# Kernel optimization log

Measured on AMD Instinct MI355X. Metric: run time of the kernel, lower is better.

The kernel has to match this reference:

```python
import jax, jax.numpy as jnp
import numpy as np
import math

T, B, D = 1024, 256, 64
E, H, L = 512, 256, 4


def setup_inputs() -> dict:
    key = jax.random.key(0)
    ks = jax.random.split(key, 10)
    x_sequence = jax.random.normal(ks[0], (T, B, D), dtype=jnp.float32)
    seq_lengths = jax.random.randint(ks[1], (B,), 1, T)
    # create_b_mask: ones in first half of dims, zeros in second half
    b_mask = jnp.concatenate([jnp.ones((1, D // 2)), jnp.zeros((1, D // 2))], axis=1).astype(jnp.float32)
    W_in = jax.random.normal(ks[2], (L, D + E, H), dtype=jnp.float32) / np.sqrt(D + E)
    b_in = jnp.zeros((L, H), dtype=jnp.float32)
    W_s = jax.random.normal(ks[3], (L, H, D), dtype=jnp.float32) / np.sqrt(H)
    b_s = jnp.zeros((L, D), dtype=jnp.float32)
    W_t = jax.random.normal(ks[4], (L, H, D), dtype=jnp.float32) / np.sqrt(H)
    b_t = jnp.zeros((L, D), dtype=jnp.float32)
    rescale_w = jnp.ones((1, D), dtype=jnp.float32)
    # ESN reservoir (fixed random), scaled for spectral stability under tanh
    W_res = jax.random.normal(ks[5], (E, E), dtype=jnp.float32) * (0.9 / np.sqrt(E))
    W_inp = jax.random.normal(ks[6], (D, E), dtype=jnp.float32) * 0.1
    return dict(x_sequence=x_sequence, seq_lengths=seq_lengths, b_mask=b_mask,
                W_in=W_in, b_in=b_in, W_s=W_s, b_s=b_s, W_t=W_t, b_t=b_t,
                rescale_w=rescale_w, W_res=W_res, W_inp=W_inp)


def _forward(x_sequence, seq_lengths, b_mask, W_in, b_in, W_s, b_s, W_t, b_t,
             rescale_w, W_res, W_inp):
    Tlen, Bsz, Dd = x_sequence.shape
    log2pi = jnp.asarray(math.log(2.0 * math.pi), dtype=x_sequence.dtype)

    def nn_apply(xm, h_esn, l):
        # small conditioning MLP: concat(masked frame, esn state) -> hidden -> (slope, intercept)
        inp = jnp.concatenate([xm, h_esn], axis=1)           # (B, D+E)
        hid = jnp.tanh(inp @ W_in[l] + b_in[l])              # (B, H)
        slope = jnp.tanh(hid @ W_s[l] + b_s[l]) * rescale_w  # (B, D), rescaled
        intercept = hid @ W_t[l] + b_t[l]                    # (B, D)
        return slope, intercept

    def f_inverse(z, m, h_esn, l):
        slope, intercept = nn_apply(m * z, h_esn, l)
        z_new = m * z + (1.0 - m) * ((z - intercept) * jnp.exp(-slope))
        log_det = slope @ (m.T - 1.0)                        # (B, 1)
        return z_new, log_det

    def loglike_frame(x_frame, h_esn):
        ll = jnp.zeros((Bsz, 1), dtype=x_frame.dtype)
        z = x_frame
        for l in reversed(range(L)):  # small fixed loop over flow layers
            z, ld = f_inverse(z, 1.0 - b_mask, h_esn, l)
            ll = ll + ld
            z, ld = f_inverse(z, b_mask, h_esn, l)
            ll = ll + ld
        ll = ll - 0.5 * jnp.sum(z * z, axis=1, keepdims=True) - 0.5 * Dd * log2pi
        return ll

    def step(carry, inp):
        h_esn, ll_seq = carry
        t, x_frame = inp
        lf = loglike_frame(x_frame, h_esn)
        length_mask = (t < seq_lengths).astype(lf.dtype)[:, None]  # (B,1)
        ll_seq = ll_seq + lf * length_mask
        h_esn = jnp.tanh(h_esn @ W_res.T + x_frame @ W_inp)        # ESN update
        return (h_esn, ll_seq), None

    h0 = jnp.zeros((Bsz, W_res.shape[0]), dtype=x_sequence.dtype)
    ll0 = jnp.zeros((Bsz, 1), dtype=x_sequence.dtype)
    ts = jnp.arange(Tlen)
    (h_final, ll_seq), _ = jax.lax.scan(step, (h0, ll0), (ts, x_sequence))
    return ll_seq  # (B, 1)


def reference(x_sequence, seq_lengths, b_mask, W_in, b_in, W_s, b_s, W_t, b_t,
              rescale_w, W_res, W_inp):
    return _forward(x_sequence, seq_lengths, b_mask, W_in, b_in, W_s, b_s,
                    W_t, b_t, rescale_w, W_res, W_inp)
```

## Files before the change

kernel.cpp:

```cpp
#include <hip/hip_runtime.h>

#define T_LEN 1024
#define B_SZ  256
#define D_DIM 64
#define E_DIM 512
#define H_DIM 256

#define SA 552
#define SH 264
#define SF 66
#define ROWB 1152

#define FLOW_LDS (32*SA*2 + 32*SH*2 + 32*4)

using short8 = __attribute__((ext_vector_type(8))) short;
using half8  = __attribute__((ext_vector_type(8))) _Float16;
using f32x4  = __attribute__((ext_vector_type(4))) float;
typedef unsigned long long ull;

static __device__ __forceinline__ unsigned short f2bf(float v) {
    unsigned u = __float_as_uint(v);
    u += 0x7FFFu + ((u >> 16) & 1u);
    return (unsigned short)(u >> 16);
}
static __device__ __forceinline__ unsigned short f2h(float v) {
    _Float16 h = (_Float16)v;
    unsigned short u;
    __builtin_memcpy(&u, &h, 2);
    return u;
}
static __device__ __forceinline__ float h2f(unsigned short u) {
    _Float16 h;
    __builtin_memcpy(&h, &u, 2);
    return (float)h;
}
static __device__ __forceinline__ float fast_tanh(float x) {
    x = fminf(15.f, fmaxf(-15.f, x));
    float e = __expf(2.f * x);
    return (e - 1.f) / (e + 1.f);
}
static __device__ __forceinline__ int rswz(int row, int byte_in_row) {
    return row * ROWB + (byte_in_row ^ ((row & 7) << 4));
}

__global__ void prep_kernel(const float* __restrict__ W_in, const float* __restrict__ W_s,
                            const float* __restrict__ W_t, const float* __restrict__ W_res,
                            const float* __restrict__ W_inp, const float* __restrict__ x_seq,
                            unsigned short* __restrict__ W_inF, unsigned short* __restrict__ W_stF,
                            unsigned short* __restrict__ W_packo, unsigned short* __restrict__ x_h) {
    int idx = blockIdx.x * blockDim.x + threadIdx.x;
    int stride = gridDim.x * blockDim.x;
    const int total1 = 8 * 16 * 17 * 64 * 8;
    for (int i = idx; i < total1; i += stride) {
        int j    = i & 7;
        int lane = (i >> 3) & 63;
        int ks   = (i >> 9) % 17;
        int nt   = (i / (512 * 17)) & 15;
        int ls   = i / (512 * 17 * 16);
        int side = ls & 1, l = ls >> 1;
        int n = nt * 16 + (lane & 15);
        int k = ks * 32 + (lane >> 4) * 8 + j;
        int ksrc = (k < 32) ? (side == 0 ? 32 + k : k) : (k + 32);
        W_inF[i] = f2bf(W_in[(l * 576 + ksrc) * H_DIM + n]);
    }
    const int total2 = 8 * 4 * 8 * 64 * 8;
    for (int i = idx; i < total2; i += stride) {
        int j    = i & 7;
        int lane = (i >> 3) & 63;
        int ks   = (i >> 9) & 7;
        int nt   = (i >> 12) & 3;
        int ls   = i >> 14;
        int side = ls & 1, l = ls >> 1;
        int nst = nt * 16 + (lane & 15);
        int k   = ks * 32 + (lane >> 4) * 8 + j;
        int j32 = nst & 31;
        int d   = side ? (32 + j32) : j32;
        float v = (nst < 32) ? W_s[(l * H_DIM + k) * D_DIM + d] : W_t[(l * H_DIM + k) * D_DIM + d];
        W_stF[i] = f2bf(v);
    }
    const int total3 = E_DIM * 576;
    for (int i = idx; i < total3; i += stride) {
        int k = i % 576;
        int n = i / 576;
        float v = (k < E_DIM) ? W_res[n * E_DIM + k] : W_inp[(k - E_DIM) * E_DIM + n];
        W_packo[i] = f2h(v);
    }
    const int total4 = T_LEN * B_SZ * D_DIM;
    for (int i = idx; i < total4; i += stride)
        x_h[i] = f2h(x_seq[i]);
}

__launch_bounds__(256, 1)
__global__ void esn_kernel(const unsigned short* __restrict__ x_h,
                           const unsigned short* __restrict__ W_pack,
                           unsigned short* __restrict__ h_store ,
                           unsigned short* __restrict__ h_buf   ,
                           unsigned int* __restrict__ ctr,
                           int t0, int tc) {
    const int bid  = blockIdx.x;
    const int g    = bid & 15;
    const int m    = bid >> 4;
    const int tid  = threadIdx.x;
    const int wave = tid >> 6;
    const int lane = tid & 63;
    const int arow = lane & 15;
    const int kq   = lane >> 4;
    const int r0   = g * 16;
    const int n0   = m * 64;
    const size_t HB = (size_t)B_SZ * E_DIM;
    unsigned int* gctr = ctr + g * 32;

    extern __shared__ char smem[];
    char* Wlb = smem;
    char* hAb = smem + 64 * ROWB;

    {
        const int r  = tid & 63;
        const int c0 = (tid >> 6) * 18;
        #pragma unroll
        for (int u = 0; u < 18; ++u) {
            const int byte = 16 * (c0 + u);
            *reinterpret_cast<uint4*>(Wlb + rswz(r, byte)) =
                *reinterpret_cast<const uint4*>(
                    reinterpret_cast<const char*>(&W_pack[(size_t)(n0 + r) * 576]) + byte);
        }
    }

    const int srow = tid >> 4;
    const int seg  = tid & 15;
    const int xrow = tid >> 2, xc = tid & 3;

    for (int tl = 0; tl < tc; ++tl) {
        const int t = t0 + tl;
        const unsigned short* hb_r = h_buf + (size_t)(t & 1) * HB;
        unsigned short*       hb_w = h_buf + (size_t)((t & 1) ^ 1) * HB;

        uint4 xa = {0,0,0,0}, xb = {0,0,0,0};
        if (tid < 64) {
            const unsigned short* xp = &x_h[((size_t)t * B_SZ + r0 + xrow) * D_DIM + xc * 16];
            xa = *reinterpret_cast<const uint4*>(xp);
            xb = *reinterpret_cast<const uint4*>(xp + 8);
        }

        if (tid == 0) {
            while (__hip_atomic_fetch_add(gctr, 0u, __ATOMIC_RELAXED,
                                          __HIP_MEMORY_SCOPE_AGENT) < 8u * (unsigned)t)
                __builtin_amdgcn_s_sleep(1);
        }
        __syncthreads();
        asm volatile("" ::: "memory");

        ull hv[8];
        const ull* hrow = reinterpret_cast<const ull*>(&hb_r[(size_t)(r0 + srow) * E_DIM]);
        #pragma unroll
        for (int q = 0; q < 4; ++q) {
            const int c = seg + 16 * q;
            hv[2*q]   = __hip_atomic_load(hrow + 2*c,     __ATOMIC_RELAXED, __HIP_MEMORY_SCOPE_SYSTEM);
            hv[2*q+1] = __hip_atomic_load(hrow + 2*c + 1, __ATOMIC_RELAXED, __HIP_MEMORY_SCOPE_SYSTEM);
        }
        #pragma unroll
        for (int q = 0; q < 4; ++q) {
            const int c = seg + 16 * q;
            uint4 pk;
            __builtin_memcpy(&pk, &hv[2*q], 16);
            *reinterpret_cast<uint4*>(hAb + rswz(srow, 16 * c)) = pk;
        }
        if (tid < 64) {
            *reinterpret_cast<uint4*>(hAb + rswz(xrow, 1024 + 32 * xc))      = xa;
            *reinterpret_cast<uint4*>(hAb + rswz(xrow, 1024 + 32 * xc + 16)) = xb;
        }
        __syncthreads();

        if (tl == 0) {
            #pragma unroll
            for (int q = 0; q < 4; ++q) {
                const int c = seg + 16 * q;
                unsigned short o[8];
                #pragma unroll
                for (int j = 0; j < 4; ++j) o[j]     = f2bf(h2f((unsigned short)(hv[2*q]   >> (16 * j))));
                #pragma unroll
                for (int j = 0; j < 4; ++j) o[4 + j] = f2bf(h2f((unsigned short)(hv[2*q+1] >> (16 * j))));
                uint4 pk;
                __builtin_memcpy(&pk, o, 16);
                *reinterpret_cast<uint4*>(&h_store[(size_t)(r0 + srow) * E_DIM + 8 * c]) = pk;
            }
        }

        f32x4 accA = (f32x4){0.f, 0.f, 0.f, 0.f};
        f32x4 accB = (f32x4){0.f, 0.f, 0.f, 0.f};
        #pragma unroll
        for (int ks = 0; ks < 18; ++ks) {
            half8 a = *reinterpret_cast<const half8*>(hAb + rswz(arow, ks * 64 + kq * 16));
            half8 b = *reinterpret_cast<const half8*>(Wlb + rswz(wave * 16 + arow, ks * 64 + kq * 16));
            if (ks & 1) accB = __builtin_amdgcn_mfma_f32_16x16x32_f16(a, b, accB, 0, 0, 0);
            else        accA = __builtin_amdgcn_mfma_f32_16x16x32_f16(a, b, accA, 0, 0, 0);
        }
        f32x4 acc = accA + accB;

        const int ncol = n0 + wave * 16 + arow;
        #pragma unroll
        for (int i = 0; i < 4; ++i) {
            const int row = r0 + kq * 4 + i;
            float hvf = fast_tanh(acc[i]);
            __hip_atomic_store(&hb_w[(size_t)row * E_DIM + ncol], f2h(hvf),
                               __ATOMIC_RELAXED, __HIP_MEMORY_SCOPE_SYSTEM);
            if (tl + 1 < tc)
                h_store[((size_t)(tl + 1) * B_SZ + row) * E_DIM + ncol] = f2bf(hvf);
        }

        asm volatile("s_waitcnt vmcnt(0)" ::: "memory");
        __syncthreads();
        if (tid == 0)
            __hip_atomic_fetch_add(gctr, 1u, __ATOMIC_RELAXED, __HIP_MEMORY_SCOPE_AGENT);
    }
}

__launch_bounds__(256, 3)
__global__ void flow_kernel(const float* __restrict__ x_seq, const unsigned short* __restrict__ h_store,
                            const unsigned short* __restrict__ W_inF, const unsigned short* __restrict__ W_stF,
                            const float* __restrict__ b_in, const float* __restrict__ b_s,
                            const float* __restrict__ b_t, const float* __restrict__ rescale_w,
                            const int* __restrict__ seq_len, float* __restrict__ ll_part,
                            int t0, int tc) {
    const int ttb  = blockIdx.x >> 4;
    const int bt   = blockIdx.x & 15;
    const int tid  = threadIdx.x;
    const int wave = tid >> 6;
    const int lane = tid & 63;

    extern __shared__ char smemf[];
    unsigned short* abf   = reinterpret_cast<unsigned short*>(smemf);
    unsigned short* hidbf = abf + 32 * SA;
    float* llacc = reinterpret_cast<float*>(hidbf + 32 * SH);
    float* stf   = reinterpret_cast<float*>(hidbf);

    const int r8 = tid >> 3;
    const int c8 = tid & 7;

    const int trow = ttb * 2 + (r8 >> 4);
    const int brow = bt * 16 + (r8 & 15);

    float z[8];
    {
        const float* xp = &x_seq[((size_t)(t0 + trow) * B_SZ + brow) * D_DIM + c8 * 8];
        float4 v0 = *reinterpret_cast<const float4*>(xp);
        float4 v1 = *reinterpret_cast<const float4*>(xp + 4);
        z[0] = v0.x; z[1] = v0.y; z[2] = v0.z; z[3] = v0.w;
        z[4] = v1.x; z[5] = v1.y; z[6] = v1.z; z[7] = v1.w;
        const unsigned short* hp = &h_store[((size_t)trow * B_SZ + brow) * E_DIM + c8 * 64];
        unsigned short* ap = &abf[r8 * SA + 32 + c8 * 64];
        #pragma unroll
        for (int q = 0; q < 8; ++q)
            *reinterpret_cast<uint4*>(ap + q * 8) = *reinterpret_cast<const uint4*>(hp + q * 8);
    }
    if (tid < 32) llacc[tid] = 0.f;
    __syncthreads();

    for (int stage = 0; stage < 8; ++stage) {
        const int l = 3 - (stage >> 1);
        const int side = stage & 1;
        const int ls = l * 2 + side;

        {
            const bool act = side ? (c8 < 4) : (c8 >= 4);
            if (act) {
                unsigned short o[8];
                #pragma unroll
                for (int q = 0; q < 8; ++q) o[q] = f2bf(z[q]);
                const int k = side ? (c8 * 8) : ((c8 - 4) * 8);
                uint4 pk;
                __builtin_memcpy(&pk, o, 16);
                *reinterpret_cast<uint4*>(&abf[r8 * SA + k]) = pk;
            }
        }
        __syncthreads();

        const unsigned short* wbase =
            W_inF + ((size_t)(ls * 16 + wave * 4) * 17) * 512 + lane * 8;
        f32x4 acc[2][4];
        #pragma unroll
        for (int mt = 0; mt < 2; ++mt)
            #pragma unroll
            for (int nt = 0; nt < 4; ++nt)
                acc[mt][nt] = (f32x4){0.f, 0.f, 0.f, 0.f};
        const int aoff = (lane & 15) * SA + 8 * (lane >> 4);
        short8 bb[6][4];
        #pragma unroll
        for (int p = 0; p < 6; ++p)
            #pragma unroll
            for (int nt = 0; nt < 4; ++nt)
                bb[p][nt] = *reinterpret_cast<const short8*>(wbase + (size_t)nt * 8704 + p * 512);
        #pragma unroll
        for (int ks = 0; ks < 17; ++ks) {
            const int k0 = ks * 32;
            short8 a0 = *reinterpret_cast<const short8*>(&abf[aoff + k0]);
            short8 a1 = *reinterpret_cast<const short8*>(&abf[16 * SA + aoff + k0]);
            #pragma unroll
            for (int nt = 0; nt < 4; ++nt) {
                acc[0][nt] = __builtin_amdgcn_mfma_f32_16x16x32_bf16(a0, bb[ks % 6][nt], acc[0][nt], 0, 0, 0);
                acc[1][nt] = __builtin_amdgcn_mfma_f32_16x16x32_bf16(a1, bb[ks % 6][nt], acc[1][nt], 0, 0, 0);
            }
            if (ks + 6 < 17) {
                #pragma unroll
                for (int nt = 0; nt < 4; ++nt)
                    bb[ks % 6][nt] = *reinterpret_cast<const short8*>(
                        wbase + (size_t)nt * 8704 + (ks + 6) * 512);
            }
        }
        #pragma unroll
        for (int mt = 0; mt < 2; ++mt)
            #pragma unroll
            for (int nt = 0; nt < 4; ++nt) {
                const int n = wave * 64 + nt * 16 + (lane & 15);
                const float bias = b_in[l * H_DIM + n];
                #pragma unroll
                for (int i = 0; i < 4; ++i) {
                    const int row = mt * 16 + (lane >> 4) * 4 + i;
                    hidbf[row * SH + n] = f2bf(fast_tanh(acc[mt][nt][i] + bias));
                }
            }
        __syncthreads();

        const unsigned short* wstb =
            W_stF + ((size_t)(ls * 4 + wave) * 8) * 512 + lane * 8;
        f32x4 acc2[2];
        acc2[0] = (f32x4){0.f,0.f,0.f,0.f};
        acc2[1] = (f32x4){0.f,0.f,0.f,0.f};
        const int hoff = (lane & 15) * SH + 8 * (lane >> 4);
        const int nst  = wave * 16 + (lane & 15);
        short8 bs0 = *reinterpret_cast<const short8*>(wstb);
        #pragma unroll
        for (int ks = 0; ks < 8; ++ks) {
            short8 bcur = bs0;
            if (ks + 1 < 8) bs0 = *reinterpret_cast<const short8*>(wstb + (ks + 1) * 512);
            const int k0 = ks * 32;
            short8 a0 = *reinterpret_cast<const short8*>(&hidbf[hoff + k0]);
            short8 a1 = *reinterpret_cast<const short8*>(&hidbf[16 * SH + hoff + k0]);
            acc2[0] = __builtin_amdgcn_mfma_f32_16x16x32_bf16(a0, bcur, acc2[0], 0, 0, 0);
            acc2[1] = __builtin_amdgcn_mfma_f32_16x16x32_bf16(a1, bcur, acc2[1], 0, 0, 0);
        }
        __syncthreads();
        {
            const int j = nst & 31;
            const int d = side ? (32 + j) : j;
            const bool is_s = (nst < 32);
            const float bias = is_s ? b_s[l * D_DIM + d] : b_t[l * D_DIM + d];
            const float rs = rescale_w[d];
            #pragma unroll
            for (int mt = 0; mt < 2; ++mt)
                #pragma unroll
                for (int i = 0; i < 4; ++i) {
                    const int row = mt * 16 + (lane >> 4) * 4 + i;
                    const float v = acc2[mt][i] + bias;
                    stf[row * SF + nst] = is_s ? (fast_tanh(v) * rs) : v;
                }
        }
        __syncthreads();
        {
            const bool act = side ? (c8 >= 4) : (c8 < 4);
            if (act) {
                const int jb = (c8 & 3) * 8;
                float p = 0.f;
                #pragma unroll
                for (int q = 0; q < 8; ++q) {
                    const float sv = stf[r8 * SF + jb + q];
                    const float iv = stf[r8 * SF + 32 + jb + q];
                    z[q] = (z[q] - iv) * __expf(-sv);
                    p += sv;
                }
                p += __shfl_xor(p, 1);
                p += __shfl_xor(p, 2);
                if ((c8 & 3) == 0) llacc[r8] -= p;
            }
        }
    }

    __syncthreads();
    {
        float zs = 0.f;
        #pragma unroll
        for (int q = 0; q < 8; ++q) zs += z[q] * z[q];
        zs += __shfl_xor(zs, 1);
        zs += __shfl_xor(zs, 2);
        zs += __shfl_xor(zs, 4);
        if (c8 == 0) {
            float ll = llacc[r8] - 0.5f * zs - 58.812066125f;
            llacc[r8] = ((t0 + trow) < seq_len[brow]) ? ll : 0.f;
        }
    }
    __syncthreads();
    if (tid < 16)
        ll_part[((size_t)((t0 >> 1) + ttb)) * B_SZ + bt * 16 + tid] =
            llacc[tid] + llacc[16 + tid];
}

__global__ void reduce_kernel(const float* __restrict__ ll_part, float* __restrict__ out) {
    int b = threadIdx.x;
    float s = 0.f;
    #pragma unroll
    for (int tt = 0; tt < T_LEN / 2; ++tt) s += ll_part[tt * B_SZ + b];
    out[b] = s;
}

extern "C" void kernel_launch(void* const* d_in, const int* in_sizes, int n_in,
                              void* d_out, int out_size, void* d_ws, size_t ws_size,
                              hipStream_t stream) {
    const float* x_seq   = (const float*)d_in[0];
    const int*   seqlen  = (const int*)d_in[1];
    const float* W_in    = (const float*)d_in[3];
    const float* b_in    = (const float*)d_in[4];
    const float* W_s     = (const float*)d_in[5];
    const float* b_s     = (const float*)d_in[6];
    const float* W_t     = (const float*)d_in[7];
    const float* b_t     = (const float*)d_in[8];
    const float* rescale = (const float*)d_in[9];
    const float* W_res   = (const float*)d_in[10];
    const float* W_inp   = (const float*)d_in[11];

    char* ws = (char*)d_ws;
    size_t off = 0;
    unsigned short* W_inF  = (unsigned short*)(ws + off); off += (size_t)8 * 16 * 17 * 64 * 8 * 2;
    unsigned short* W_stF  = (unsigned short*)(ws + off); off += (size_t)8 * 4 * 8 * 64 * 8 * 2;
    unsigned short* W_pack = (unsigned short*)(ws + off); off += (size_t)E_DIM * 576 * 2;
    unsigned short* x_h    = (unsigned short*)(ws + off); off += (size_t)T_LEN * B_SZ * D_DIM * 2;
    float* ll_part = (float*)(ws + off); off += (size_t)(T_LEN / 2) * B_SZ * 4;
    unsigned short* h_buf  = (unsigned short*)(ws + off); off += (size_t)2 * B_SZ * E_DIM * 2;
    unsigned int* ctr = (unsigned int*)(ws + off); off += (size_t)16 * 32 * 4;
    unsigned short* h_store = (unsigned short*)(ws + off);

    size_t per_t = (size_t)B_SZ * E_DIM * 2;
    size_t rem = (ws_size > off) ? (ws_size - off) : 0;
    long long tcl = (long long)(rem / per_t);
    int tc = (int)((tcl > T_LEN) ? T_LEN : tcl);
    tc &= ~15;
    if (tc < 16) tc = 16;

    hipMemsetAsync(h_buf, 0, (size_t)2 * B_SZ * E_DIM * 2, stream);
    hipMemsetAsync(ctr, 0, (size_t)16 * 32 * 4, stream);

    prep_kernel<<<2048, 256, 0, stream>>>(W_in, W_s, W_t, W_res, W_inp, x_seq,
                                          W_inF, W_stF, W_pack, x_h);
    const int esn_lds = (64 + 16) * ROWB;
    for (int t0 = 0; t0 < T_LEN; t0 += tc) {
        int cur = T_LEN - t0; if (cur > tc) cur = tc;
        esn_kernel<<<128, 256, esn_lds, stream>>>(x_h, W_pack, h_store, h_buf, ctr, t0, cur);
        flow_kernel<<<(cur / 2) * 16, 256, FLOW_LDS, stream>>>(x_seq, h_store, W_inF, W_stF,
                                                               b_in, b_s, b_t, rescale, seqlen,
                                                               ll_part, t0, cur);
    }
    reduce_kernel<<<1, B_SZ, 0, stream>>>(ll_part, (float*)d_out);
}
```

Before: 3.615 ms.

## Interleave two row groups per ESN block to hide cross-block sync latency

Each ESN workgroup now handles two 16-row batch groups instead of one, and the grid shrinks from 128 to 64 blocks. The block alternates between the groups: while it computes the MFMA and tanh for one group, it waits on the counter and loads the next h state and x frame for the other. This is meant to hide the latency of the global spin-wait and the h_buf loads behind useful compute on the recurrent critical path. The cost is half as many blocks, so each block does twice the serial work, plus a more complex vmcnt-based wait scheme that could deadlock or read stale data if the ordering assumptions are wrong.

```diff
diff --git a/kernel.cpp b/kernel.cpp
--- a/kernel.cpp
+++ b/kernel.cpp
@@ -12,6 +12,7 @@
 #define ROWB 1152
 
 #define FLOW_LDS (32*SA*2 + 32*SH*2 + 32*4)
+#define ESN_LDS  (96*ROWB)
 
 using short8 = __attribute__((ext_vector_type(8))) short;
 using half8  = __attribute__((ext_vector_type(8))) _Float16;
@@ -90,6 +91,96 @@
         x_h[i] = f2h(x_seq[i]);
 }
 
+static __device__ __forceinline__ void esn_phase(
+        char* ha, char* Wlb, int r0x, unsigned int* gcx,
+        ull (&hvx)[8], uint2& xvx,
+        int r0o, unsigned int* gco, ull (&hvo)[8], uint2& xvo,
+        int t, int tl, int tc, int tread, bool do_reads,
+        const unsigned short* __restrict__ x_h,
+        unsigned short* __restrict__ h_store,
+        unsigned short* __restrict__ h_buf,
+        int tid, int wave, int lane, int n0) {
+    const int arow = lane & 15;
+    const int kq   = lane >> 4;
+    const int srow = tid >> 4;
+    const int seg  = tid & 15;
+    const size_t HB = (size_t)B_SZ * E_DIM;
+
+    #pragma unroll
+    for (int qq = 0; qq < 4; ++qq) {
+        const int c = seg + 16 * qq;
+        uint4 pk;
+        __builtin_memcpy(&pk, &hvx[2 * qq], 16);
+        *reinterpret_cast<uint4*>(ha + rswz(srow, 16 * c)) = pk;
+    }
+    *reinterpret_cast<uint2*>(ha + rswz(srow, 1024 + seg * 8)) = xvx;
+    __syncthreads();
+
+    if (tl == 0) {
+        #pragma unroll
+        for (int qq = 0; qq < 4; ++qq) {
+            const int c = seg + 16 * qq;
+            unsigned short o[8];
+            #pragma unroll
+            for (int j = 0; j < 4; ++j) o[j]     = f2bf(h2f((unsigned short)(hvx[2*qq]   >> (16 * j))));
+            #pragma unroll
+            for (int j = 0; j < 4; ++j) o[4 + j] = f2bf(h2f((unsigned short)(hvx[2*qq+1] >> (16 * j))));
+            uint4 pk;
+            __builtin_memcpy(&pk, o, 16);
+            *reinterpret_cast<uint4*>(&h_store[(size_t)(r0x + srow) * E_DIM + 8 * c]) = pk;
+        }
+    }
+
+    f32x4 accA = (f32x4){0.f, 0.f, 0.f, 0.f};
+    f32x4 accB = (f32x4){0.f, 0.f, 0.f, 0.f};
+    #pragma unroll
+    for (int ks = 0; ks < 18; ++ks) {
+        half8 a = *reinterpret_cast<const half8*>(ha + rswz(arow, ks * 64 + kq * 16));
+        half8 b = *reinterpret_cast<const half8*>(Wlb + rswz(wave * 16 + arow, ks * 64 + kq * 16));
+        if (ks & 1) accB = __builtin_amdgcn_mfma_f32_16x16x32_f16(a, b, accB, 0, 0, 0);
+        else        accA = __builtin_amdgcn_mfma_f32_16x16x32_f16(a, b, accA, 0, 0, 0);
+    }
+    f32x4 acc = accA + accB;
+
+    unsigned short* hb_w = h_buf + (size_t)((t + 1) & 1) * HB;
+    const int ncol = n0 + wave * 16 + arow;
+    #pragma unroll
+    for (int i = 0; i < 4; ++i) {
+        const int row = r0x + kq * 4 + i;
+        float hvf = fast_tanh(acc[i]);
+        __hip_atomic_store(&hb_w[(size_t)row * E_DIM + ncol], f2h(hvf),
+                           __ATOMIC_RELAXED, __HIP_MEMORY_SCOPE_SYSTEM);
+        if (tl + 1 < tc)
+            h_store[((size_t)(tl + 1) * B_SZ + row) * E_DIM + ncol] = f2bf(hvf);
+    }
+
+    if (do_reads) {
+        if (tid == 0) {
+            while (__hip_atomic_fetch_add(gco, 0u, __ATOMIC_RELAXED,
+                                          __HIP_MEMORY_SCOPE_AGENT) < 8u * (unsigned)tread)
+                __builtin_amdgcn_s_sleep(1);
+        }
+        __syncthreads();
+        asm volatile("" ::: "memory");
+        const unsigned short* hb_r = h_buf + (size_t)(tread & 1) * HB;
+        const ull* hrow = reinterpret_cast<const ull*>(&hb_r[(size_t)(r0o + srow) * E_DIM]);
+        #pragma unroll
+        for (int qq = 0; qq < 4; ++qq) {
+            const int c = seg + 16 * qq;
+            hvo[2*qq]   = __hip_atomic_load(hrow + 2*c,     __ATOMIC_RELAXED, __HIP_MEMORY_SCOPE_SYSTEM);
+            hvo[2*qq+1] = __hip_atomic_load(hrow + 2*c + 1, __ATOMIC_RELAXED, __HIP_MEMORY_SCOPE_SYSTEM);
+        }
+        xvo = *reinterpret_cast<const uint2*>(
+            &x_h[((size_t)tread * B_SZ + r0o + srow) * D_DIM + seg * 4]);
+        asm volatile("s_waitcnt vmcnt(9)" ::: "memory");
+    } else {
+        asm volatile("s_waitcnt vmcnt(0)" ::: "memory");
+    }
+    __syncthreads();
+    if (tid == 0)
+        __hip_atomic_fetch_add(gcx, 1u, __ATOMIC_RELAXED, __HIP_MEMORY_SCOPE_AGENT);
+}
+
 __launch_bounds__(256, 1)
 __global__ void esn_kernel(const unsigned short* __restrict__ x_h,
                            const unsigned short* __restrict__ W_pack,
@@ -98,21 +189,23 @@
                            unsigned int* __restrict__ ctr,
                            int t0, int tc) {
     const int bid  = blockIdx.x;
-    const int g    = bid & 15;
-    const int m    = bid >> 4;
+    const int q    = bid & 7;
+    const int m    = bid >> 3;
     const int tid  = threadIdx.x;
     const int wave = tid >> 6;
     const int lane = tid & 63;
-    const int arow = lane & 15;
-    const int kq   = lane >> 4;
-    const int r0   = g * 16;
     const int n0   = m * 64;
     const size_t HB = (size_t)B_SZ * E_DIM;
-    unsigned int* gctr = ctr + g * 32;
+
+    const int r0A = (q * 2) * 16;
+    const int r0B = (q * 2 + 1) * 16;
+    unsigned int* gcA = ctr + (q * 2) * 32;
+    unsigned int* gcB = ctr + (q * 2 + 1) * 32;
 
     extern __shared__ char smem[];
-    char* Wlb = smem;
-    char* hAb = smem + 64 * ROWB;
+    char* Wlb  = smem;
+    char* hAbA = smem + 64 * ROWB;
+    char* hAbB = smem + 80 * ROWB;
 
     {
         const int r  = tid & 63;
@@ -128,90 +221,40 @@
 
     const int srow = tid >> 4;
     const int seg  = tid & 15;
-    const int xrow = tid >> 2, xc = tid & 3;
+
+    ull hvA[8], hvB[8];
+    uint2 xvA, xvB;
+
+    if (tid == 0) {
+        while (__hip_atomic_fetch_add(gcA, 0u, __ATOMIC_RELAXED,
+                                      __HIP_MEMORY_SCOPE_AGENT) < 8u * (unsigned)t0)
+            __builtin_amdgcn_s_sleep(1);
+    }
+    __syncthreads();
+    asm volatile("" ::: "memory");
+    {
+        const unsigned short* hb_r = h_buf + (size_t)(t0 & 1) * HB;
+        const ull* hrow = reinterpret_cast<const ull*>(&hb_r[(size_t)(r0A + srow) * E_DIM]);
+        #pragma unroll
+        for (int qq = 0; qq < 4; ++qq) {
+            const int c = seg + 16 * qq;
+            hvA[2*qq]   = __hip_atomic_load(hrow + 2*c,     __ATOMIC_RELAXED, __HIP_MEMORY_SCOPE_SYSTEM);
+            hvA[2*qq+1] = __hip_atomic_load(hrow + 2*c + 1, __ATOMIC_RELAXED, __HIP_MEMORY_SCOPE_SYSTEM);
+        }
+        xvA = *reinterpret_cast<const uint2*>(
+            &x_h[((size_t)t0 * B_SZ + r0A + srow) * D_DIM + seg * 4]);
+    }
 
     for (int tl = 0; tl < tc; ++tl) {
         const int t = t0 + tl;
-        const unsigned short* hb_r = h_buf + (size_t)(t & 1) * HB;
-        unsigned short*       hb_w = h_buf + (size_t)((t & 1) ^ 1) * HB;
-
-        uint4 xa = {0,0,0,0}, xb = {0,0,0,0};
-        if (tid < 64) {
-            const unsigned short* xp = &x_h[((size_t)t * B_SZ + r0 + xrow) * D_DIM + xc * 16];
-            xa = *reinterpret_cast<const uint4*>(xp);
-            xb = *reinterpret_cast<const uint4*>(xp + 8);
-        }
-
-        if (tid == 0) {
-            while (__hip_atomic_fetch_add(gctr, 0u, __ATOMIC_RELAXED,
-                                          __HIP_MEMORY_SCOPE_AGENT) < 8u * (unsigned)t)
-                __builtin_amdgcn_s_sleep(1);
-        }
-        __syncthreads();
-        asm volatile("" ::: "memory");
-
-        ull hv[8];
-        const ull* hrow = reinterpret_cast<const ull*>(&hb_r[(size_t)(r0 + srow) * E_DIM]);
-        #pragma unroll
-        for (int q = 0; q < 4; ++q) {
-            const int c = seg + 16 * q;
-            hv[2*q]   = __hip_atomic_load(hrow + 2*c,     __ATOMIC_RELAXED, __HIP_MEMORY_SCOPE_SYSTEM);
-            hv[2*q+1] = __hip_atomic_load(hrow + 2*c + 1, __ATOMIC_RELAXED, __HIP_MEMORY_SCOPE_SYSTEM);
-        }
-        #pragma unroll
-        for (int q = 0; q < 4; ++q) {
-            const int c = seg + 16 * q;
-            uint4 pk;
-            __builtin_memcpy(&pk, &hv[2*q], 16);
-            *reinterpret_cast<uint4*>(hAb + rswz(srow, 16 * c)) = pk;
-        }
-        if (tid < 64) {
-            *reinterpret_cast<uint4*>(hAb + rswz(xrow, 1024 + 32 * xc))      = xa;
-            *reinterpret_cast<uint4*>(hAb + rswz(xrow, 1024 + 32 * xc + 16)) = xb;
-        }
-        __syncthreads();
-
-        if (tl == 0) {
-            #pragma unroll
-            for (int q = 0; q < 4; ++q) {
-                const int c = seg + 16 * q;
-                unsigned short o[8];
-                #pragma unroll
-                for (int j = 0; j < 4; ++j) o[j]     = f2bf(h2f((unsigned short)(hv[2*q]   >> (16 * j))));
-                #pragma unroll
-                for (int j = 0; j < 4; ++j) o[4 + j] = f2bf(h2f((unsigned short)(hv[2*q+1] >> (16 * j))));
-                uint4 pk;
-                __builtin_memcpy(&pk, o, 16);
-                *reinterpret_cast<uint4*>(&h_store[(size_t)(r0 + srow) * E_DIM + 8 * c]) = pk;
-            }
-        }
-
-        f32x4 accA = (f32x4){0.f, 0.f, 0.f, 0.f};
-        f32x4 accB = (f32x4){0.f, 0.f, 0.f, 0.f};
-        #pragma unroll
-        for (int ks = 0; ks < 18; ++ks) {
-            half8 a = *reinterpret_cast<const half8*>(hAb + rswz(arow, ks * 64 + kq * 16));
-            half8 b = *reinterpret_cast<const half8*>(Wlb + rswz(wave * 16 + arow, ks * 64 + kq * 16));
-            if (ks & 1) accB = __builtin_amdgcn_mfma_f32_16x16x32_f16(a, b, accB, 0, 0, 0);
-            else        accA = __builtin_amdgcn_mfma_f32_16x16x32_f16(a, b, accA, 0, 0, 0);
-        }
-        f32x4 acc = accA + accB;
-
-        const int ncol = n0 + wave * 16 + arow;
-        #pragma unroll
-        for (int i = 0; i < 4; ++i) {
-            const int row = r0 + kq * 4 + i;
-            float hvf = fast_tanh(acc[i]);
-            __hip_atomic_store(&hb_w[(size_t)row * E_DIM + ncol], f2h(hvf),
-                               __ATOMIC_RELAXED, __HIP_MEMORY_SCOPE_SYSTEM);
-            if (tl + 1 < tc)
-                h_store[((size_t)(tl + 1) * B_SZ + row) * E_DIM + ncol] = f2bf(hvf);
-        }
-
-        asm volatile("s_waitcnt vmcnt(0)" ::: "memory");
-        __syncthreads();
-        if (tid == 0)
-            __hip_atomic_fetch_add(gctr, 1u, __ATOMIC_RELAXED, __HIP_MEMORY_SCOPE_AGENT);
+        esn_phase(hAbA, Wlb, r0A, gcA, hvA, xvA,
+                  r0B, gcB, hvB, xvB,
+                  t, tl, tc, t, true,
+                  x_h, h_store, h_buf, tid, wave, lane, n0);
+        esn_phase(hAbB, Wlb, r0B, gcB, hvB, xvB,
+                  r0A, gcA, hvA, xvA,
+                  t, tl, tc, t + 1, (tl + 1 < tc),
+                  x_h, h_store, h_buf, tid, wave, lane, n0);
     }
 }
 
@@ -440,10 +483,9 @@
 
     prep_kernel<<<2048, 256, 0, stream>>>(W_in, W_s, W_t, W_res, W_inp, x_seq,
                                           W_inF, W_stF, W_pack, x_h);
-    const int esn_lds = (64 + 16) * ROWB;
     for (int t0 = 0; t0 < T_LEN; t0 += tc) {
         int cur = T_LEN - t0; if (cur > tc) cur = tc;
-        esn_kernel<<<128, 256, esn_lds, stream>>>(x_h, W_pack, h_store, h_buf, ctr, t0, cur);
+        esn_kernel<<<64, 256, ESN_LDS, stream>>>(x_h, W_pack, h_store, h_buf, ctr, t0, cur);
         flow_kernel<<<(cur / 2) * 16, 256, FLOW_LDS, stream>>>(x_seq, h_store, W_inF, W_stF,
                                                                b_in, b_s, b_t, rescale, seqlen,
                                                                ll_part, t0, cur);
```

Result: slower. 4.878 ms (+34.9%).
